# Kernel tuning notes

Hardware: AMD Instinct MI355X
Metric: run time of the kernel (lower is better)

The kernel has to match this reference:

```python
import jax, jax.numpy as jnp
import numpy as np

B, C, H, W = 4, 64, 96, 320
K = 9  # 3x3 kernel points
EPS = 1e-5


def conv3x3(x, w, b):
    # x: [B,Cin,H,W], w: [Cout,Cin,3,3], stride 1, pad 1
    out = jax.lax.conv_general_dilated(
        x, w, window_strides=(1, 1), padding=[(1, 1), (1, 1)],
        dimension_numbers=("NCHW", "OIHW", "NCHW"))
    return out + b[None, :, None, None]


def bn_eval(x, gamma, beta, mean, var):
    scale = gamma / jnp.sqrt(var + EPS)
    return x * scale[None, :, None, None] + (beta - mean * scale)[None, :, None, None]


def mdcn(x, offset, mask, w, b):
    # Modulated deformable conv v2, kernel 3, stride 1, pad 1, dilation 1.
    # offset: [B,2K,H,W] (channel 2k = dy, 2k+1 = dx, mmcv layout); mask: [B,K,H,W]
    Bb, Cc, Hh, Ww = x.shape
    off = offset.reshape(Bb, K, 2, Hh, Ww)
    dy, dx = off[:, :, 0], off[:, :, 1]               # [B,K,H,W]
    ks = jnp.arange(K)
    ky = (ks // 3 - 1).astype(x.dtype)[None, :, None, None]  # kernel row offset (pad=1)
    kx = (ks % 3 - 1).astype(x.dtype)[None, :, None, None]
    py = jnp.arange(Hh, dtype=x.dtype)[None, None, :, None] + ky + dy  # sample y
    px = jnp.arange(Ww, dtype=x.dtype)[None, None, None, :] + kx + dx  # sample x
    y0 = jnp.floor(py); x0 = jnp.floor(px)
    wy = py - y0; wx = px - x0
    y0i = y0.astype(jnp.int32); x0i = x0.astype(jnp.int32)
    x_flat = x.reshape(Bb, Cc, Hh * Ww)

    def gather(yi, xi):
        # bilinear corner with zero padding outside the image
        valid = ((yi >= 0) & (yi < Hh) & (xi >= 0) & (xi < Ww)).astype(x.dtype)
        idx = (jnp.clip(yi, 0, Hh - 1) * Ww + jnp.clip(xi, 0, Ww - 1)).reshape(Bb, 1, K * Hh * Ww)
        v = jnp.take_along_axis(x_flat, idx, axis=2).reshape(Bb, Cc, K, Hh, Ww)
        return v * valid[:, None]

    val = (((1 - wy) * (1 - wx))[:, None] * gather(y0i, x0i)
           + ((1 - wy) * wx)[:, None] * gather(y0i, x0i + 1)
           + (wy * (1 - wx))[:, None] * gather(y0i + 1, x0i)
           + (wy * wx)[:, None] * gather(y0i + 1, x0i + 1))  # [B,C,K,H,W]
    val = val * mask[:, None]
    out = jnp.einsum('bckhw,ock->bohw', val, w.reshape(w.shape[0], Cc, K))
    return out + b[None, :, None, None]


def setup_inputs() -> dict:
    key = jax.random.key(0)
    ks = jax.random.split(key, 16)
    s = 0.05
    return {
        "feat_rgb": jax.random.normal(ks[0], (B, C, H, W), jnp.float32),
        "feat_depth": jax.random.normal(ks[1], (B, C, H, W), jnp.float32),
        "w_off1": jax.random.normal(ks[2], (C, C, 3, 3), jnp.float32) * s,
        "b_off1": jax.random.normal(ks[3], (C,), jnp.float32) * s,
        "g1": 1.0 + jax.random.normal(ks[4], (C,), jnp.float32) * 0.1,
        "be1": jax.random.normal(ks[5], (C,), jnp.float32) * 0.1,
        "m1": jax.random.normal(ks[6], (C,), jnp.float32) * 0.1,
        "v1": jax.random.uniform(ks[7], (C,), jnp.float32, 0.5, 1.5),
        "w_off2": jax.random.normal(ks[8], (3 * K, C, 3, 3), jnp.float32) * s,
        "b_off2": jax.random.normal(ks[9], (3 * K,), jnp.float32) * s,
        "w_def": jax.random.normal(ks[10], (C, C, 3, 3), jnp.float32) * s,
        "b_def": jax.random.normal(ks[11], (C,), jnp.float32) * s,
        "w_f1": jax.random.normal(ks[12], (C, 2 * C, 3, 3), jnp.float32) * s,
        "b_f1": jax.random.normal(ks[13], (C,), jnp.float32) * s,
        "g2": 1.0 + jax.random.normal(ks[14], (C,), jnp.float32) * 0.1,
        "be2": jax.random.normal(ks[15], (C,), jnp.float32) * 0.1,
        "m2": jax.random.normal(jax.random.fold_in(key, 101), (C,), jnp.float32) * 0.1,
        "v2": jax.random.uniform(jax.random.fold_in(key, 102), (C,), jnp.float32, 0.5, 1.5),
        "w_out": jax.random.normal(jax.random.fold_in(key, 103), (1, C, 3, 3), jnp.float32) * s,
        "b_out": jax.random.normal(jax.random.fold_in(key, 104), (1,), jnp.float32) * s,
    }


def reference(feat_rgb, feat_depth, w_off1, b_off1, g1, be1, m1, v1,
              w_off2, b_off2, w_def, b_def, w_f1, b_f1, g2, be2, m2, v2,
              w_out, b_out):
    # offset head
    t = conv3x3(feat_rgb, w_off1, b_off1)
    t = bn_eval(t, g1, be1, m1, v1)
    head = conv3x3(t, w_off2, b_off2)            # [B,27,H,W]
    o1, o2, msk = jnp.split(head, 3, axis=1)
    offset = jnp.concatenate([o1, o2], axis=1)   # [B,18,H,W]
    msk = jax.nn.sigmoid(msk)                    # [B,9,H,W]
    # modulated deformable conv on depth features
    deform = mdcn(feat_depth, offset, msk, w_def, b_def)
    fd = feat_depth + deform
    fusion = jnp.concatenate([fd, feat_rgb], axis=1)  # [B,2C,H,W]
    h = jax.nn.relu(fusion)
    h = conv3x3(h, w_f1, b_f1)
    h = bn_eval(h, g2, be2, m2, v2)
    h = jax.nn.relu(h)  # Dropout(0.1) is identity at eval
    return conv3x3(h, w_out, b_out)  # [B,1,H,W]
```

## Files before the change

kernel.cpp:

```cpp
#include <hip/hip_runtime.h>
#include <math.h>

constexpr int Bc  = 4;
constexpr int Hc  = 96;
constexpr int Wc  = 320;
constexpr int HWc = Hc * Wc;
constexpr int NPIX = Bc * HWc;

typedef __attribute__((ext_vector_type(8))) short short8;
typedef __attribute__((ext_vector_type(4))) float f32x4;

constexpr size_t B_W1   = 0;
constexpr size_t B_W2   = 73728;
constexpr size_t B_WD   = 110592;
constexpr size_t B_WF   = 184320;
constexpr size_t B_AB   = 331776;
constexpr size_t B_RGBT = 332800;
constexpr size_t B_DEPT = 16061440;
constexpr size_t B_TT   = 31790080;
constexpr size_t B_HEAD = 47518720;

static __device__ __forceinline__ unsigned short f2bf(float f) {
    unsigned u = __builtin_bit_cast(unsigned, f);
    u = (u + 0x7fffu + ((u >> 16) & 1u)) >> 16;
    return (unsigned short)u;
}
static __device__ __forceinline__ float bf2f(unsigned short h) {
    unsigned u = ((unsigned)h) << 16;
    return __builtin_bit_cast(float, u);
}
static __device__ __forceinline__ int swz_blk(int bid, int chunk) {
    return (bid & 7) * chunk + (bid >> 3);
}

__global__ void prep_w(const float* __restrict__ w1, const float* __restrict__ b1,
                       const float* __restrict__ g1, const float* __restrict__ be1,
                       const float* __restrict__ m1, const float* __restrict__ v1,
                       const float* __restrict__ w2,
                       const float* __restrict__ wd,
                       const float* __restrict__ wf, const float* __restrict__ bf1,
                       const float* __restrict__ g2, const float* __restrict__ be2,
                       const float* __restrict__ m2, const float* __restrict__ v2,
                       char* __restrict__ ws) {
    int tid = blockIdx.x * blockDim.x + threadIdx.x;
    int stride = gridDim.x * blockDim.x;
    unsigned short* W1 = (unsigned short*)(ws + B_W1);
    unsigned short* W2 = (unsigned short*)(ws + B_W2);
    unsigned short* WD = (unsigned short*)(ws + B_WD);
    unsigned short* WF = (unsigned short*)(ws + B_WF);
    float* AB = (float*)(ws + B_AB);
    for (int i = tid; i < 36864; i += stride) {
        int ci = i & 63, co = (i >> 6) & 63, kk = i >> 12;
        W1[i] = f2bf(w1[(co * 64 + ci) * 9 + kk]);
    }
    for (int i = tid; i < 18432; i += stride) {
        int ci = i & 63, co = (i >> 6) & 31, kk = i >> 11;
        W2[i] = (co < 27) ? f2bf(w2[(co * 64 + ci) * 9 + kk]) : (unsigned short)0;
    }
    for (int i = tid; i < 36864; i += stride) {
        int c = i & 63, o = (i >> 6) & 63, kk = i >> 12;
        WD[i] = f2bf(wd[(o * 64 + c) * 9 + kk]);
    }
    for (int i = tid; i < 73728; i += stride) {
        int ci = i & 63, co = (i >> 6) & 63, r = i >> 12;
        int kk = r % 9, h = r / 9;
        WF[i] = f2bf(wf[(co * 128 + h * 64 + ci) * 9 + kk]);
    }
    if (tid < 64) {
        float s1 = g1[tid] / sqrtf(v1[tid] + 1e-5f);
        AB[tid]        = s1;
        AB[64 + tid]   = b1[tid] * s1 + be1[tid] - m1[tid] * s1;
        float s2 = g2[tid] / sqrtf(v2[tid] + 1e-5f);
        AB[128 + tid]  = s2;
        AB[192 + tid]  = bf1[tid] * s2 + be2[tid] - m2[tid] * s2;
    }
}

__global__ __launch_bounds__(256) void prep_x(const float* __restrict__ rgb,
                                              const float* __restrict__ dep,
                                              unsigned short* __restrict__ rgbT,
                                              unsigned short* __restrict__ depT) {
    int i = blockIdx.x * 256 + threadIdx.x;
    if (i >= NPIX * 8) return;
    int g = i & 7;
    int pg = i >> 3;
    int b = pg / HWc, p = pg % HWc;
    size_t sb = (size_t)b * 64 * HWc + p + (size_t)(g * 8) * HWc;
    unsigned short r8[8], d8[8];
#pragma unroll
    for (int j = 0; j < 8; ++j) {
        r8[j] = f2bf(rgb[sb + (size_t)j * HWc]);
        d8[j] = f2bf(dep[sb + (size_t)j * HWc]);
    }
    *(short8*)(rgbT + (size_t)pg * 64 + g * 8) = *(short8*)r8;
    *(short8*)(depT + (size_t)pg * 64 + g * 8) = *(short8*)d8;
}

static __device__ __forceinline__ void stage6(const unsigned short* __restrict__ src,
                                              int b, int y0, int x0,
                                              unsigned short* lds, bool do_relu) {
#pragma unroll
    for (int it = 0; it < 13; ++it) {
        int i = threadIdx.x + it * 256;
        if (i < 3168) {
            int g = i & 7;
            int xx = (i >> 3) % 66;
            int row = (i >> 3) / 66;
            int y = y0 - 1 + row, x = x0 - 1 + xx;
            short8 v = (short8)0;
            if ((unsigned)y < 96u && (unsigned)x < 320u) {
                v = *(const short8*)(src + ((size_t)(b * HWc + y * Wc + x)) * 64 + g * 8);
            }
            if (do_relu) {
#pragma unroll
                for (int j = 0; j < 8; ++j) {
                    short s = v[j];
                    v[j] = (s & (short)0x8000) ? (short)0 : s;
                }
            }
            int byte = ((row * 66 + xx) * 64 + g * 8) * 2;
            byte ^= ((xx & 7) << 4);
            *(short8*)((char*)lds + byte) = v;
        }
    }
}

static __device__ __forceinline__ short8 read_b6(const unsigned short* lds, int row, int xx, int cofs) {
    int byte = ((row * 66 + xx) * 64 + cofs) * 2;
    byte ^= ((xx & 7) << 4);
    return *(const short8*)((const char*)lds + byte);
}

__global__ __launch_bounds__(256) void conv1_m(const unsigned short* __restrict__ rgbT,
                                               const char* __restrict__ ws,
                                               unsigned short* __restrict__ tT) {
    __shared__ __align__(16) unsigned short xls[6 * 66 * 64];
    const unsigned short* W1 = (const unsigned short*)(ws + B_W1);
    const float* AB = (const float*)(ws + B_AB);
    int blk = swz_blk(blockIdx.x, 60);
    int xt = blk % 5, yt = (blk / 5) % 24, b = blk / 120;
    int x0 = xt * 64, y0 = yt * 4;
    stage6(rgbT, b, y0, x0, xls, false);
    __syncthreads();
    int lane = threadIdx.x & 63, w = threadIdx.x >> 6;
    int pl = lane & 15, q4 = lane >> 4;
    int p = w * 16 + pl;
    f32x4 acc[4][4];
#pragma unroll
    for (int r = 0; r < 4; ++r)
#pragma unroll
        for (int cp = 0; cp < 4; ++cp) acc[r][cp] = (f32x4)0.f;
#pragma unroll
    for (int kk = 0; kk < 9; ++kk) {
        int dy = kk / 3, dx = kk % 3;
        int xx = p + dx;
#pragma unroll
        for (int ch = 0; ch < 2; ++ch) {
            short8 bfr[4];
#pragma unroll
            for (int r = 0; r < 4; ++r) bfr[r] = read_b6(xls, dy + r, xx, ch * 32 + q4 * 8);
#pragma unroll
            for (int cp = 0; cp < 4; ++cp) {
                short8 afr = *(const short8*)(W1 + ((kk * 64 + cp * 16 + pl) * 64 + ch * 32 + q4 * 8));
#pragma unroll
                for (int r = 0; r < 4; ++r)
                    acc[r][cp] = __builtin_amdgcn_mfma_f32_16x16x32_bf16(afr, bfr[r], acc[r][cp], 0, 0, 0);
            }
        }
    }
#pragma unroll
    for (int r = 0; r < 4; ++r) {
        size_t pglob = (size_t)(b * HWc + (y0 + r) * Wc + x0 + p);
#pragma unroll
        for (int cp = 0; cp < 4; ++cp) {
            int co0 = cp * 16 + q4 * 4;
            f32x4 a1 = *(const f32x4*)(AB + co0);
            f32x4 b1 = *(const f32x4*)(AB + 64 + co0);
            unsigned short h4[4];
#pragma unroll
            for (int j = 0; j < 4; ++j) h4[j] = f2bf(fmaf(acc[r][cp][j], a1[j], b1[j]));
            uint2 u;
            u.x = (unsigned)h4[0] | ((unsigned)h4[1] << 16);
            u.y = (unsigned)h4[2] | ((unsigned)h4[3] << 16);
            *(uint2*)(tT + pglob * 64 + co0) = u;
        }
    }
}

__global__ __launch_bounds__(256) void conv2_m(const char* __restrict__ ws,
                                               const float* __restrict__ b2,
                                               float* __restrict__ headT,
                                               const unsigned short* __restrict__ tT) {
    __shared__ __align__(16) unsigned short xls[6 * 66 * 64];
    const unsigned short* W2 = (const unsigned short*)(ws + B_W2);
    int blk = swz_blk(blockIdx.x, 60);
    int xt = blk % 5, yt = (blk / 5) % 24, b = blk / 120;
    int x0 = xt * 64, y0 = yt * 4;
    stage6(tT, b, y0, x0, xls, false);
    __syncthreads();
    int lane = threadIdx.x & 63, w = threadIdx.x >> 6;
    int pl = lane & 15, q4 = lane >> 4;
    int p = w * 16 + pl;
    f32x4 acc[4][2];
#pragma unroll
    for (int r = 0; r < 4; ++r) { acc[r][0] = (f32x4)0.f; acc[r][1] = (f32x4)0.f; }
#pragma unroll
    for (int kk = 0; kk < 9; ++kk) {
        int dy = kk / 3, dx = kk % 3;
        int xx = p + dx;
#pragma unroll
        for (int ch = 0; ch < 2; ++ch) {
            short8 bfr[4];
#pragma unroll
            for (int r = 0; r < 4; ++r) bfr[r] = read_b6(xls, dy + r, xx, ch * 32 + q4 * 8);
#pragma unroll
            for (int cp = 0; cp < 2; ++cp) {
                short8 afr = *(const short8*)(W2 + ((kk * 32 + cp * 16 + pl) * 64 + ch * 32 + q4 * 8));
#pragma unroll
                for (int r = 0; r < 4; ++r)
                    acc[r][cp] = __builtin_amdgcn_mfma_f32_16x16x32_bf16(afr, bfr[r], acc[r][cp], 0, 0, 0);
            }
        }
    }
#pragma unroll
    for (int r = 0; r < 4; ++r) {
        size_t pglob = (size_t)(b * HWc + (y0 + r) * Wc + x0 + p);
#pragma unroll
        for (int cp = 0; cp < 2; ++cp) {
            int co0 = cp * 16 + q4 * 4;
            f32x4 rr;
#pragma unroll
            for (int j = 0; j < 4; ++j) {
                float bias = (co0 + j < 27) ? b2[co0 + j] : 0.f;
                rr[j] = acc[r][cp][j] + bias;
            }
            *(f32x4*)(headT + pglob * 32 + co0) = rr;
        }
    }
}

__global__ __launch_bounds__(256) void mdcn_r(const float* __restrict__ feat_depth,
                                              const unsigned short* __restrict__ depthT,
                                              const float* __restrict__ headT,
                                              const char* __restrict__ ws,
                                              const float* __restrict__ bd,
                                              unsigned short* __restrict__ fdreluT) {
    const unsigned short* WD = (const unsigned short*)(ws + B_WD);
    int blk = swz_blk(blockIdx.x, 240);
    int xt = blk % 5, y = (blk / 5) % 96, b = blk / 480;
    int x0 = xt * 64;
    int lane = threadIdx.x & 63, w = threadIdx.x >> 6;
    int pl = lane & 15, q4 = lane >> 4;
    int p = w * 16 + pl;
    int px = x0 + p;
    size_t pglob = (size_t)(b * HWc + y * Wc + px);
    size_t dbase = (size_t)b * HWc * 64;
    const float* hd = headT + pglob * 32;
    float hv[28];
#pragma unroll
    for (int i = 0; i < 7; ++i) {
        f32x4 t = *(const f32x4*)(hd + i * 4);
        hv[i * 4 + 0] = t[0]; hv[i * 4 + 1] = t[1];
        hv[i * 4 + 2] = t[2]; hv[i * 4 + 3] = t[3];
    }
    f32x4 acc[4];
#pragma unroll
    for (int cp = 0; cp < 4; ++cp) acc[cp] = (f32x4)0.f;

    int   o_[2][4];
    float w_[2][4];
    short8 f_[2][8];

#define MPARAMS(KK, S) {                                                      \
    float dyv = hv[2*(KK)], dxv = hv[2*(KK)+1], sm = hv[18+(KK)];             \
    float m = 1.f / (1.f + __expf(-sm));                                      \
    float py  = (float)(y + (KK)/3 - 1) + dyv;                                \
    float pxf = (float)(px + (KK)%3 - 1) + dxv;                               \
    float y0f = floorf(py), x0f = floorf(pxf);                                \
    float wy = py - y0f, wx = pxf - x0f;                                      \
    int iy0 = (int)y0f, ix0 = (int)x0f;                                       \
    bool vy0 = (unsigned)iy0 < 96u, vy1 = (unsigned)(iy0+1) < 96u;            \
    bool vx0 = (unsigned)ix0 < 320u, vx1 = (unsigned)(ix0+1) < 320u;          \
    int cy0 = min(max(iy0,0),95),  cy1 = min(max(iy0+1,0),95);                \
    int cx0 = min(max(ix0,0),319), cx1 = min(max(ix0+1,0),319);               \
    w_[S][0] = (vy0 && vx0) ? (1.f-wy)*(1.f-wx)*m : 0.f;                      \
    w_[S][1] = (vy0 && vx1) ? (1.f-wy)*wx*m : 0.f;                            \
    w_[S][2] = (vy1 && vx0) ? wy*(1.f-wx)*m : 0.f;                            \
    w_[S][3] = (vy1 && vx1) ? wy*wx*m : 0.f;                                  \
    o_[S][0] = cy0*Wc+cx0; o_[S][1] = cy0*Wc+cx1;                             \
    o_[S][2] = cy1*Wc+cx0; o_[S][3] = cy1*Wc+cx1; }

#define MISSUE(S) {                                                           \
    const unsigned short* bp = depthT + dbase + q4 * 8;                       \
    _Pragma("unroll")                                                         \
    for (int c = 0; c < 4; ++c) {                                             \
        const unsigned short* rp = bp + (size_t)o_[S][c] * 64;                \
        f_[S][c*2+0] = *(const short8*)(rp);                                  \
        f_[S][c*2+1] = *(const short8*)(rp + 32);                             \
    } }

    MPARAMS(0, 0)
    MISSUE(0)
#pragma unroll
    for (int kk = 0; kk < 9; ++kk) {
        int cur = kk & 1, nxt = cur ^ 1;
        if (kk < 8) {
            MPARAMS(kk + 1, nxt)
            MISSUE(nxt)
        }
#pragma unroll
        for (int ch = 0; ch < 2; ++ch) {
            unsigned short vv[8];
#pragma unroll
            for (int j = 0; j < 8; ++j) {
                float v = w_[cur][0] * bf2f((unsigned short)f_[cur][0*2+ch][j])
                        + w_[cur][1] * bf2f((unsigned short)f_[cur][1*2+ch][j])
                        + w_[cur][2] * bf2f((unsigned short)f_[cur][2*2+ch][j])
                        + w_[cur][3] * bf2f((unsigned short)f_[cur][3*2+ch][j]);
                vv[j] = f2bf(v);
            }
            short8 bfr = *(short8*)vv;
#pragma unroll
            for (int cp = 0; cp < 4; ++cp) {
                short8 afr = *(const short8*)(WD + ((kk * 64 + cp * 16 + pl) * 64 + ch * 32 + q4 * 8));
                acc[cp] = __builtin_amdgcn_mfma_f32_16x16x32_bf16(afr, bfr, acc[cp], 0, 0, 0);
            }
        }
    }
#undef MPARAMS
#undef MISSUE
    int pix = y * Wc + px;
#pragma unroll
    for (int cp = 0; cp < 4; ++cp) {
        int co0 = cp * 16 + q4 * 4;
        f32x4 bdv = *(const f32x4*)(bd + co0);
        unsigned short h4[4];
#pragma unroll
        for (int j = 0; j < 4; ++j) {
            float r = acc[cp][j] + bdv[j] + feat_depth[((size_t)b * 64 + co0 + j) * HWc + pix];
            h4[j] = f2bf(fmaxf(r, 0.f));
        }
        uint2 u;
        u.x = (unsigned)h4[0] | ((unsigned)h4[1] << 16);
        u.y = (unsigned)h4[2] | ((unsigned)h4[3] << 16);
        *(uint2*)(fdreluT + ((size_t)(b * HWc) + pix) * 64 + co0) = u;
    }
}

__global__ __launch_bounds__(256) void convf_m(const unsigned short* __restrict__ fdreluT,
                                               const unsigned short* __restrict__ rgbT,
                                               const char* __restrict__ ws,
                                               unsigned short* __restrict__ hT) {
    __shared__ __align__(16) unsigned short xls[6 * 66 * 64];
    const unsigned short* WF = (const unsigned short*)(ws + B_WF);
    const float* AB = (const float*)(ws + B_AB);
    int blk = swz_blk(blockIdx.x, 60);
    int xt = blk % 5, yt = (blk / 5) % 24, b = blk / 120;
    int x0 = xt * 64, y0 = yt * 4;
    int lane = threadIdx.x & 63, w = threadIdx.x >> 6;
    int pl = lane & 15, q4 = lane >> 4;
    int p = w * 16 + pl;
    f32x4 acc[4][4];
#pragma unroll
    for (int r = 0; r < 4; ++r)
#pragma unroll
        for (int cp = 0; cp < 4; ++cp) acc[r][cp] = (f32x4)0.f;
#pragma unroll
    for (int half = 0; half < 2; ++half) {
        if (half) __syncthreads();
        stage6(half ? rgbT : fdreluT, b, y0, x0, xls, half != 0);
        __syncthreads();
        const unsigned short* Wh = WF + half * 36864;
#pragma unroll
        for (int kk = 0; kk < 9; ++kk) {
            int dy = kk / 3, dx = kk % 3;
            int xx = p + dx;
#pragma unroll
            for (int ch = 0; ch < 2; ++ch) {
                short8 bfr[4];
#pragma unroll
                for (int r = 0; r < 4; ++r) bfr[r] = read_b6(xls, dy + r, xx, ch * 32 + q4 * 8);
#pragma unroll
                for (int cp = 0; cp < 4; ++cp) {
                    short8 afr = *(const short8*)(Wh + ((kk * 64 + cp * 16 + pl) * 64 + ch * 32 + q4 * 8));
#pragma unroll
                    for (int r = 0; r < 4; ++r)
                        acc[r][cp] = __builtin_amdgcn_mfma_f32_16x16x32_bf16(afr, bfr[r], acc[r][cp], 0, 0, 0);
                }
            }
        }
    }
#pragma unroll
    for (int r = 0; r < 4; ++r) {
        size_t pglob = (size_t)(b * HWc + (y0 + r) * Wc + x0 + p);
#pragma unroll
        for (int cp = 0; cp < 4; ++cp) {
            int co0 = cp * 16 + q4 * 4;
            f32x4 a2 = *(const f32x4*)(AB + 128 + co0);
            f32x4 b2 = *(const f32x4*)(AB + 192 + co0);
            unsigned short h4[4];
#pragma unroll
            for (int j = 0; j < 4; ++j) h4[j] = f2bf(fmaxf(fmaf(acc[r][cp][j], a2[j], b2[j]), 0.f));
            uint2 u;
            u.x = (unsigned)h4[0] | ((unsigned)h4[1] << 16);
            u.y = (unsigned)h4[2] | ((unsigned)h4[3] << 16);
            *(uint2*)(hT + pglob * 64 + co0) = u;
        }
    }
}

__global__ __launch_bounds__(256) void convo_m(const unsigned short* __restrict__ hT,
                                               const float* __restrict__ wo,
                                               const float* __restrict__ bo,
                                               float* __restrict__ out) {
    __shared__ float wl[576];
    for (int i = threadIdx.x; i < 576; i += 256) wl[i] = wo[i];
    __syncthreads();
    int p = swz_blk(blockIdx.x, 60) * 256 + threadIdx.x;
    int xw = p % Wc, rem = p / Wc, y = rem % Hc, b = rem / Hc;
    float acc = bo[0];
#pragma unroll
    for (int kk = 0; kk < 9; ++kk) {
        int iy = y + kk / 3 - 1, ix = xw + kk % 3 - 1;
        if ((unsigned)iy < 96u && (unsigned)ix < 320u) {
            const unsigned short* base = hT + ((size_t)(b * HWc + iy * Wc + ix)) * 64;
#pragma unroll
            for (int g = 0; g < 8; ++g) {
                short8 v = *(const short8*)(base + g * 8);
#pragma unroll
                for (int j = 0; j < 8; ++j)
                    acc = fmaf(bf2f((unsigned short)v[j]), wl[(g * 8 + j) * 9 + kk], acc);
            }
        }
    }
    out[p] = acc;
}

extern "C" void kernel_launch(void* const* d_in, const int* in_sizes, int n_in,
                              void* d_out, int out_size, void* d_ws, size_t ws_size,
                              hipStream_t stream) {
    const float* feat_rgb   = (const float*)d_in[0];
    const float* feat_depth = (const float*)d_in[1];
    const float* w_off1 = (const float*)d_in[2];
    const float* b_off1 = (const float*)d_in[3];
    const float* g1  = (const float*)d_in[4];
    const float* be1 = (const float*)d_in[5];
    const float* m1  = (const float*)d_in[6];
    const float* v1  = (const float*)d_in[7];
    const float* w_off2 = (const float*)d_in[8];
    const float* b_off2 = (const float*)d_in[9];
    const float* w_def  = (const float*)d_in[10];
    const float* b_def  = (const float*)d_in[11];
    const float* w_f1   = (const float*)d_in[12];
    const float* b_f1   = (const float*)d_in[13];
    const float* g2  = (const float*)d_in[14];
    const float* be2 = (const float*)d_in[15];
    const float* m2  = (const float*)d_in[16];
    const float* v2  = (const float*)d_in[17];
    const float* w_out = (const float*)d_in[18];
    const float* b_out = (const float*)d_in[19];
    (void)in_sizes; (void)n_in; (void)out_size; (void)ws_size;

    char* ws = (char*)d_ws;
    unsigned short* rgbT   = (unsigned short*)(ws + B_RGBT);
    unsigned short* depthT = (unsigned short*)(ws + B_DEPT);
    unsigned short* tT     = (unsigned short*)(ws + B_TT);
    float*          headT  = (float*)(ws + B_HEAD);
    unsigned short* fdreluT = tT;
    unsigned short* hT      = depthT;

    prep_w<<<64, 256, 0, stream>>>(w_off1, b_off1, g1, be1, m1, v1,
                                   w_off2, w_def, w_f1, b_f1, g2, be2, m2, v2, ws);
    prep_x<<<(NPIX * 8 + 255) / 256, 256, 0, stream>>>(feat_rgb, feat_depth, rgbT, depthT);
    conv1_m<<<480, 256, 0, stream>>>(rgbT, ws, tT);
    conv2_m<<<480, 256, 0, stream>>>(ws, b_off2, headT, tT);
    mdcn_r <<<1920, 256, 0, stream>>>(feat_depth, depthT, headT, ws, b_def, fdreluT);
    convf_m<<<480, 256, 0, stream>>>(fdreluT, rgbT, ws, hT);
    convo_m<<<480, 256, 0, stream>>>(hT, w_out, b_out, (float*)d_out);
}
```

Measured before the change: 409.2 us.

## Stage depth window in LDS for deformable conv bilinear gathers

The modulated deformable conv kernel now loads an 11x74-pixel halo window of bf16 depth features into shared memory. It does this in two channel-half passes, then takes the bilinear corner samples from LDS, falling back to global loads only for samples that land outside the window. The residual add also reads the bf16 transposed depth tensor instead of strided fp32 feat_depth, which lowers precision slightly. The aim is to replace scattered global and cache gathers with LDS reads. The cost is a large cooperative window load for each one-row tile, about 52KB of LDS that limits occupancy, extra barriers, and the loss of the previous register double-buffered prefetch.

```diff
diff --git a/kernel.cpp b/kernel.cpp
--- a/kernel.cpp
+++ b/kernel.cpp
@@ -239,12 +239,12 @@
     }
 }
 
-__global__ __launch_bounds__(256) void mdcn_r(const float* __restrict__ feat_depth,
-                                              const unsigned short* __restrict__ depthT,
+__global__ __launch_bounds__(256) void mdcn_l(const unsigned short* __restrict__ depthT,
                                               const float* __restrict__ headT,
                                               const char* __restrict__ ws,
                                               const float* __restrict__ bd,
                                               unsigned short* __restrict__ fdreluT) {
+    __shared__ __align__(16) unsigned short vls[26048];
     const unsigned short* WD = (const unsigned short*)(ws + B_WD);
     int blk = swz_blk(blockIdx.x, 240);
     int xt = blk % 5, y = (blk / 5) % 96, b = blk / 480;
@@ -267,83 +267,94 @@
 #pragma unroll
     for (int cp = 0; cp < 4; ++cp) acc[cp] = (f32x4)0.f;
 
-    int   o_[2][4];
-    float w_[2][4];
-    short8 f_[2][8];
-
-#define MPARAMS(KK, S) {                                                      \
-    float dyv = hv[2*(KK)], dxv = hv[2*(KK)+1], sm = hv[18+(KK)];             \
-    float m = 1.f / (1.f + __expf(-sm));                                      \
-    float py  = (float)(y + (KK)/3 - 1) + dyv;                                \
-    float pxf = (float)(px + (KK)%3 - 1) + dxv;                               \
-    float y0f = floorf(py), x0f = floorf(pxf);                                \
-    float wy = py - y0f, wx = pxf - x0f;                                      \
-    int iy0 = (int)y0f, ix0 = (int)x0f;                                       \
-    bool vy0 = (unsigned)iy0 < 96u, vy1 = (unsigned)(iy0+1) < 96u;            \
-    bool vx0 = (unsigned)ix0 < 320u, vx1 = (unsigned)(ix0+1) < 320u;          \
-    int cy0 = min(max(iy0,0),95),  cy1 = min(max(iy0+1,0),95);                \
-    int cx0 = min(max(ix0,0),319), cx1 = min(max(ix0+1,0),319);               \
-    w_[S][0] = (vy0 && vx0) ? (1.f-wy)*(1.f-wx)*m : 0.f;                      \
-    w_[S][1] = (vy0 && vx1) ? (1.f-wy)*wx*m : 0.f;                            \
-    w_[S][2] = (vy1 && vx0) ? wy*(1.f-wx)*m : 0.f;                            \
-    w_[S][3] = (vy1 && vx1) ? wy*wx*m : 0.f;                                  \
-    o_[S][0] = cy0*Wc+cx0; o_[S][1] = cy0*Wc+cx1;                             \
-    o_[S][2] = cy1*Wc+cx0; o_[S][3] = cy1*Wc+cx1; }
-
-#define MISSUE(S) {                                                           \
-    const unsigned short* bp = depthT + dbase + q4 * 8;                       \
-    _Pragma("unroll")                                                         \
-    for (int c = 0; c < 4; ++c) {                                             \
-        const unsigned short* rp = bp + (size_t)o_[S][c] * 64;                \
-        f_[S][c*2+0] = *(const short8*)(rp);                                  \
-        f_[S][c*2+1] = *(const short8*)(rp + 32);                             \
-    } }
-
-    MPARAMS(0, 0)
-    MISSUE(0)
-#pragma unroll
-    for (int kk = 0; kk < 9; ++kk) {
-        int cur = kk & 1, nxt = cur ^ 1;
-        if (kk < 8) {
-            MPARAMS(kk + 1, nxt)
-            MISSUE(nxt)
-        }
-#pragma unroll
-        for (int ch = 0; ch < 2; ++ch) {
+    const int wy0 = y - 5;
+    const int wx0 = x0 - 5;
+
+#pragma unroll
+    for (int pass = 0; pass < 2; ++pass) {
+        if (pass) __syncthreads();
+#pragma unroll
+        for (int it = 0; it < 13; ++it) {
+            int i = threadIdx.x + it * 256;
+            if (i < 3256) {
+                int sub = i & 3;
+                int c = (i >> 2) % 74;
+                int r = (i >> 2) / 74;
+                int gy = wy0 + r, gx = wx0 + c;
+                short8 v = (short8)0;
+                if ((unsigned)gy < 96u && (unsigned)gx < 320u)
+                    v = *(const short8*)(depthT + ((size_t)(b * HWc + gy * Wc + gx)) * 64 + pass * 32 + sub * 8);
+                int byte = (((r * 74 + c) * 64) + sub * 16) ^ ((c & 6) << 3);
+                *(short8*)((char*)vls + byte) = v;
+            }
+        }
+        __syncthreads();
+#pragma unroll
+        for (int kk = 0; kk < 9; ++kk) {
+            float dyv = hv[2 * kk], dxv = hv[2 * kk + 1], sm = hv[18 + kk];
+            float m = 1.f / (1.f + __expf(-sm));
+            float py  = (float)(y + kk / 3 - 1) + dyv;
+            float pxf = (float)(px + kk % 3 - 1) + dxv;
+            float y0f = floorf(py), x0f = floorf(pxf);
+            float wy = py - y0f, wx = pxf - x0f;
+            int iy0 = (int)y0f, ix0 = (int)x0f;
+            bool vy0 = (unsigned)iy0 < 96u, vy1 = (unsigned)(iy0 + 1) < 96u;
+            bool vx0 = (unsigned)ix0 < 320u, vx1 = (unsigned)(ix0 + 1) < 320u;
+            int cy0 = min(max(iy0, 0), 95),  cy1 = min(max(iy0 + 1, 0), 95);
+            int cx0 = min(max(ix0, 0), 319), cx1 = min(max(ix0 + 1, 0), 319);
+            float w00 = (vy0 && vx0) ? (1.f - wy) * (1.f - wx) * m : 0.f;
+            float w01 = (vy0 && vx1) ? (1.f - wy) * wx * m : 0.f;
+            float w10 = (vy1 && vx0) ? wy * (1.f - wx) * m : 0.f;
+            float w11 = (vy1 && vx1) ? wy * wx * m : 0.f;
+            bool inw = ((unsigned)(iy0 - wy0) <= 9u) && ((unsigned)(ix0 - wx0) <= 72u);
+            int lr0 = min(max(cy0 - wy0, 0), 10), lr1 = min(max(cy1 - wy0, 0), 10);
+            int lc0 = min(max(cx0 - wx0, 0), 73), lc1 = min(max(cx1 - wx0, 0), 73);
+            int qb = q4 * 16;
+            short8 f00 = *(const short8*)((const char*)vls + ((((lr0 * 74 + lc0) * 64) + qb) ^ ((lc0 & 6) << 3)));
+            short8 f01 = *(const short8*)((const char*)vls + ((((lr0 * 74 + lc1) * 64) + qb) ^ ((lc1 & 6) << 3)));
+            short8 f10 = *(const short8*)((const char*)vls + ((((lr1 * 74 + lc0) * 64) + qb) ^ ((lc0 & 6) << 3)));
+            short8 f11 = *(const short8*)((const char*)vls + ((((lr1 * 74 + lc1) * 64) + qb) ^ ((lc1 & 6) << 3)));
+            if (!__all(inw)) {
+                if (!inw) {
+                    const unsigned short* bp = depthT + dbase + pass * 32 + q4 * 8;
+                    f00 = *(const short8*)(bp + (size_t)(cy0 * Wc + cx0) * 64);
+                    f01 = *(const short8*)(bp + (size_t)(cy0 * Wc + cx1) * 64);
+                    f10 = *(const short8*)(bp + (size_t)(cy1 * Wc + cx0) * 64);
+                    f11 = *(const short8*)(bp + (size_t)(cy1 * Wc + cx1) * 64);
+                }
+            }
             unsigned short vv[8];
 #pragma unroll
             for (int j = 0; j < 8; ++j) {
-                float v = w_[cur][0] * bf2f((unsigned short)f_[cur][0*2+ch][j])
-                        + w_[cur][1] * bf2f((unsigned short)f_[cur][1*2+ch][j])
-                        + w_[cur][2] * bf2f((unsigned short)f_[cur][2*2+ch][j])
-                        + w_[cur][3] * bf2f((unsigned short)f_[cur][3*2+ch][j]);
+                float v = w00 * bf2f((unsigned short)f00[j]) + w01 * bf2f((unsigned short)f01[j])
+                        + w10 * bf2f((unsigned short)f10[j]) + w11 * bf2f((unsigned short)f11[j]);
                 vv[j] = f2bf(v);
             }
             short8 bfr = *(short8*)vv;
 #pragma unroll
             for (int cp = 0; cp < 4; ++cp) {
-                short8 afr = *(const short8*)(WD + ((kk * 64 + cp * 16 + pl) * 64 + ch * 32 + q4 * 8));
+                short8 afr = *(const short8*)(WD + ((kk * 64 + cp * 16 + pl) * 64 + pass * 32 + q4 * 8));
                 acc[cp] = __builtin_amdgcn_mfma_f32_16x16x32_bf16(afr, bfr, acc[cp], 0, 0, 0);
             }
         }
     }
-#undef MPARAMS
-#undef MISSUE
-    int pix = y * Wc + px;
 #pragma unroll
     for (int cp = 0; cp < 4; ++cp) {
         int co0 = cp * 16 + q4 * 4;
         f32x4 bdv = *(const f32x4*)(bd + co0);
+        uint2 dres = *(const uint2*)(depthT + pglob * 64 + co0);
+        unsigned short d4[4] = { (unsigned short)(dres.x & 0xffff), (unsigned short)(dres.x >> 16),
+                                 (unsigned short)(dres.y & 0xffff), (unsigned short)(dres.y >> 16) };
         unsigned short h4[4];
 #pragma unroll
         for (int j = 0; j < 4; ++j) {
-            float r = acc[cp][j] + bdv[j] + feat_depth[((size_t)b * 64 + co0 + j) * HWc + pix];
+            float r = acc[cp][j] + bdv[j] + bf2f(d4[j]);
             h4[j] = f2bf(fmaxf(r, 0.f));
         }
         uint2 u;
         u.x = (unsigned)h4[0] | ((unsigned)h4[1] << 16);
         u.y = (unsigned)h4[2] | ((unsigned)h4[3] << 16);
-        *(uint2*)(fdreluT + ((size_t)(b * HWc) + pix) * 64 + co0) = u;
+        *(uint2*)(fdreluT + pglob * 64 + co0) = u;
     }
 }
 
@@ -474,7 +485,7 @@
     prep_x<<<(NPIX * 8 + 255) / 256, 256, 0, stream>>>(feat_rgb, feat_depth, rgbT, depthT);
     conv1_m<<<480, 256, 0, stream>>>(rgbT, ws, tT);
     conv2_m<<<480, 256, 0, stream>>>(ws, b_off2, headT, tT);
-    mdcn_r <<<1920, 256, 0, stream>>>(feat_depth, depthT, headT, ws, b_def, fdreluT);
+    mdcn_l <<<1920, 256, 0, stream>>>(depthT, headT, ws, b_def, fdreluT);
     convf_m<<<480, 256, 0, stream>>>(fdreluT, rgbT, ws, hT);
     convo_m<<<480, 256, 0, stream>>>(hT, w_out, b_out, (float*)d_out);
 }
```

Result: faster. 396.4 us (-3.1%).
